# Kernel optimization log

Hardware: AMD Instinct MI355X
Metric: run time of the kernel (lower is better)

The kernel has to match this reference:

```python
import jax, jax.numpy as jnp
import numpy as np
import math

LEVELS = 10
T = 4096              # 2**log2_hashmap_size, log2=12
F = 2                 # n_features_per_level
NMIN, NMAX = 16, 320
HIDDEN = 512
OMEGA = 30.0
COOR_DIM = LEVELS * F + 2   # 22: hash feats + raw coords
_b = math.exp((math.log(NMAX) - math.log(NMIN)) / (LEVELS - 1))
RES = [int(math.floor(NMIN * _b ** l)) for l in range(LEVELS)]
PRIME_Y = np.uint32(2654435761)
MASK = np.uint32(T - 1)


def _hash2(xi, yi):
    # instant-NGP style spatial hash for 2D, uint32 wraparound arithmetic
    return (xi ^ (yi * PRIME_Y)) & MASK


def hash_encode(coords, table):
    # coords: [N,2] in [0,1); table: [LEVELS, T, F]
    feats = []
    for l in range(LEVELS):
        x = coords * RES[l]               # [N,2] continuous grid coords
        x0 = jnp.floor(x)
        w = x - x0                        # bilinear weights in [0,1)
        xi = x0.astype(jnp.uint32)
        x0i, y0i = xi[:, 0], xi[:, 1]
        x1i, y1i = x0i + np.uint32(1), y0i + np.uint32(1)
        tab = table[l]
        f00 = tab[_hash2(x0i, y0i)]       # [N,F] gathers
        f10 = tab[_hash2(x1i, y0i)]
        f01 = tab[_hash2(x0i, y1i)]
        f11 = tab[_hash2(x1i, y1i)]
        wx = w[:, 0:1]
        wy = w[:, 1:2]
        fx0 = f00 + (f10 - f00) * wx
        fx1 = f01 + (f11 - f01) * wx
        feats.append(fx0 + (fx1 - fx0) * wy)
    return jnp.concatenate(feats + [coords], axis=-1)  # [N, COOR_DIM]


def sine(x, w, b):
    # SineLayer.forward: sin(linear(x)); omega_0 is baked into first-layer init
    return jnp.sin(x @ w.T + b)


def _sine_init(key, out_f, in_f, is_first):
    kw, kb = jax.random.split(key)
    if is_first:
        lim = OMEGA / in_f
    else:
        lim = math.sqrt(6.0 / in_f) / OMEGA
    w = jax.random.uniform(kw, (out_f, in_f), jnp.float32, -lim, lim)
    blim = 1.0 / math.sqrt(in_f)
    b = jax.random.uniform(kb, (out_f,), jnp.float32, -blim, blim)
    return w, b


def setup_inputs() -> dict:
    key = jax.random.key(0)
    ks = jax.random.split(key, 8)
    N = 262144
    coords = jax.random.uniform(ks[0], (N, 2), jnp.float32)
    table = jax.random.uniform(ks[1], (LEVELS, T, F), jnp.float32, -1e-4, 1e-4)
    w1, b1 = _sine_init(ks[2], HIDDEN, COOR_DIM, True)
    w2, b2 = _sine_init(ks[3], HIDDEN, HIDDEN, False)
    ws1, bs1 = _sine_init(ks[4], HIDDEN, COOR_DIM + HIDDEN, False)
    ws2, bs2 = _sine_init(ks[5], HIDDEN, HIDDEN, False)
    wo, bo = _sine_init(ks[6], 2, HIDDEN, False)
    return {"coords": coords, "table": table,
            "w1": w1, "b1": b1, "w2": w2, "b2": b2,
            "ws1": ws1, "bs1": bs1, "ws2": ws2, "bs2": bs2,
            "wo": wo, "bo": bo}


def reference(coords, table, w1, b1, w2, b2, ws1, bs1, ws2, bs2, wo, bo):
    h0 = hash_encode(coords, table)            # [N,22]
    h1 = sine(sine(h0, w1, b1), w2, b2)        # first block (n_flayer=2)
    h2 = jnp.concatenate([h1, h0], axis=-1)    # skip connection [N,534]
    h2 = sine(sine(h2, ws1, bs1), ws2, bs2)    # second block (n_slayer=2)
    return sine(h2, wo, bo)                    # [N,2]
```

## Files before the change

### kernel.cpp

```cpp
#include <hip/hip_runtime.h>
#include <hip/hip_bf16.h>
#include <math.h>

#define MBLK    64
#define H0_OFF  65536
#define LDSB    (H0_OFF + 64*64)

#define OFF_W1  0
#define OFF_W2  16384
#define OFF_WS1 (16384+262144)
#define OFF_WS2 (278528+278528)
#define OFF_WO  (557056+262144)
#define NPACK   (819200+1024)

typedef __attribute__((ext_vector_type(8))) short bf16x8;
typedef __attribute__((ext_vector_type(4))) float f32x4;

struct ResArr { int r[10]; };

__device__ __forceinline__ unsigned short f2bf(float f) {
    unsigned u = __float_as_uint(f);
    u += 0x7FFFu + ((u >> 16) & 1u);
    return (unsigned short)(u >> 16);
}
__device__ __forceinline__ float bf2f(unsigned short h) {
    return __uint_as_float(((unsigned)h) << 16);
}

__global__ void pack_weights(const float* __restrict__ w1, const float* __restrict__ w2,
                             const float* __restrict__ ws1, const float* __restrict__ ws2,
                             const float* __restrict__ wo, unsigned short* __restrict__ out)
{
    int i = blockIdx.x * 256 + threadIdx.x;
    if (i >= NPACK) return;
    float v;
    if (i < OFF_WO) {
        int il, KC, K_src, K_valid;
        const float* src;
        if (i < OFF_W2)       { il = i;           KC = 1;  K_src = 22;  K_valid = 22;  src = w1;  }
        else if (i < OFF_WS1) { il = i - OFF_W2;  KC = 16; K_src = 512; K_valid = 512; src = w2;  }
        else if (i < OFF_WS2) { il = i - OFF_WS1; KC = 17; K_src = 534; K_valid = 534; src = ws1; }
        else                  { il = i - OFF_WS2; KC = 16; K_src = 512; K_valid = 512; src = ws2; }
        int blk  = il >> 9, idx = il & 511;
        int lane = idx >> 3, j = idx & 7;
        int nf   = blk & 3;
        int rest = blk >> 2;
        int c    = rest % KC;
        int nb   = rest / KC;
        int n = nb * 64 + nf * 16 + (lane & 15);
        int k = c * 32 + (lane >> 4) * 8 + j;
        v = (k < K_valid) ? src[n * K_src + k] : 0.f;
    } else {
        v = wo[i - OFF_WO];
    }
    out[i] = f2bf(v);
}

template<int KSTEPS, bool TAIL, bool PREBAR>
__device__ __forceinline__ void mlp_layer(char* sm, const unsigned short* __restrict__ Wl,
                                          const float* __restrict__ bias,
                                          int wid, int lane)
{
    constexpr int NC = KSTEPS + (TAIL ? 1 : 0);
    const int n0 = wid * 64;
    const int lm = lane & 15;
    const int lk = lane >> 4;
    const int xm = lm << 4;

    const unsigned short* wnb = Wl + (unsigned)(wid * NC) * 2048 + (lane << 3);

    f32x4 acc[4][4];
    #pragma unroll
    for (int i = 0; i < 4; ++i)
        #pragma unroll
        for (int j = 0; j < 4; ++j) { f32x4 z = {0.f,0.f,0.f,0.f}; acc[i][j] = z; }

    #pragma unroll 1
    for (int ks = 0; ks < KSTEPS; ++ks) {
        bf16x8 w[4], a[4];
        #pragma unroll
        for (int nf = 0; nf < 4; ++nf)
            w[nf] = *(const bf16x8*)(wnb + ((ks*4 + nf) << 9));
        #pragma unroll
        for (int mf = 0; mf < 4; ++mf)
            a[mf] = *(const bf16x8*)(sm + ((((mf*16 + lm) << 10) + ks*64 + lk*16) ^ xm));
        #pragma unroll
        for (int mf = 0; mf < 4; ++mf)
            #pragma unroll
            for (int nf = 0; nf < 4; ++nf)
                acc[mf][nf] = __builtin_amdgcn_mfma_f32_16x16x32_bf16(w[nf], a[mf], acc[mf][nf], 0, 0, 0);
    }
    if (TAIL) {
        bf16x8 w[4], a[4];
        #pragma unroll
        for (int nf = 0; nf < 4; ++nf)
            w[nf] = *(const bf16x8*)(wnb + ((KSTEPS*4 + nf) << 9));
        #pragma unroll
        for (int mf = 0; mf < 4; ++mf)
            a[mf] = *(const bf16x8*)(sm + H0_OFF + ((((mf*16 + lm) << 6) + lk*16) ^ ((lm & 7) << 4)));
        #pragma unroll
        for (int mf = 0; mf < 4; ++mf)
            #pragma unroll
            for (int nf = 0; nf < 4; ++nf)
                acc[mf][nf] = __builtin_amdgcn_mfma_f32_16x16x32_bf16(w[nf], a[mf], acc[mf][nf], 0, 0, 0);
    }

    if (PREBAR) __syncthreads();

    #pragma unroll
    for (int nf = 0; nf < 4; ++nf) {
        const float4 bv = *(const float4*)(bias + n0 + nf*16 + lk*4);
        const int colb = (n0 + nf*16 + lk*4) * 2;
        #pragma unroll
        for (int mf = 0; mf < 4; ++mf) {
            float s0 = __sinf(acc[mf][nf][0] + bv.x);
            float s1 = __sinf(acc[mf][nf][1] + bv.y);
            float s2 = __sinf(acc[mf][nf][2] + bv.z);
            float s3 = __sinf(acc[mf][nf][3] + bv.w);
            uint2 pk;
            pk.x = (unsigned)f2bf(s0) | ((unsigned)f2bf(s1) << 16);
            pk.y = (unsigned)f2bf(s2) | ((unsigned)f2bf(s3) << 16);
            int row = mf*16 + lm;
            *(uint2*)(sm + (((row << 10) + colb) ^ xm)) = pk;
        }
    }
    __syncthreads();
}

__global__ __launch_bounds__(512) __attribute__((amdgpu_waves_per_eu(4))) void siren_fused(
    const float* __restrict__ coords, const float* __restrict__ table,
    const float* __restrict__ b1, const float* __restrict__ b2,
    const float* __restrict__ bs1, const float* __restrict__ bs2,
    const float* __restrict__ bo,
    const unsigned short* __restrict__ Wp,
    float* __restrict__ outp,
    ResArr res)
{
    extern __shared__ char sm[];
    const int tid = threadIdx.x;
    const int pbase = blockIdx.x * MBLK;

    {
        int p  = tid & 63;
        int lg = tid >> 6;
        float2 cc = ((const float2*)coords)[pbase + p];
        #pragma unroll
        for (int li = 0; li < 2; ++li) {
            int l = lg + 8 * li;
            if (l < 10) {
                float R  = (float)res.r[l];
                float fx = cc.x * R, fy = cc.y * R;
                float x0 = floorf(fx), y0 = floorf(fy);
                float wx = fx - x0,  wy = fy - y0;
                unsigned xi = (unsigned)x0, yi = (unsigned)y0;
                unsigned yp  = yi * 2654435761u;
                unsigned yp1 = (yi + 1u) * 2654435761u;
                unsigned h00 = (xi        ^ yp ) & 4095u;
                unsigned h10 = ((xi + 1u) ^ yp ) & 4095u;
                unsigned h01 = (xi        ^ yp1) & 4095u;
                unsigned h11 = ((xi + 1u) ^ yp1) & 4095u;
                const float2* tl = (const float2*)(table + l * 8192);
                float2 f00 = tl[h00], f10 = tl[h10], f01 = tl[h01], f11 = tl[h11];
                float a0 = f00.x + (f10.x - f00.x) * wx;
                float a1 = f01.x + (f11.x - f01.x) * wx;
                float g0 = a0 + (a1 - a0) * wy;
                float c0 = f00.y + (f10.y - f00.y) * wx;
                float c1 = f01.y + (f11.y - f01.y) * wx;
                float g1 = c0 + (c1 - c0) * wy;
                unsigned pk = (unsigned)f2bf(g0) | ((unsigned)f2bf(g1) << 16);
                *(unsigned*)(sm + H0_OFF + (((p << 6) + 4*l) ^ ((p & 7) << 4))) = pk;
            }
        }
        if (lg == 2) {
            unsigned pk = (unsigned)f2bf(cc.x) | ((unsigned)f2bf(cc.y) << 16);
            *(unsigned*)(sm + H0_OFF + (((p << 6) + 40) ^ ((p & 7) << 4))) = pk;
        }
        if (lg == 3) {
            #pragma unroll
            for (int bb = 44; bb < 64; bb += 4)
                *(unsigned*)(sm + H0_OFF + (((p << 6) + bb) ^ ((p & 7) << 4))) = 0u;
        }
    }
    __syncthreads();

    const int wid  = tid >> 6;
    const int lane = tid & 63;

    mlp_layer<0,  true,  false>(sm, Wp + OFF_W1,  b1,  wid, lane);
    mlp_layer<16, false, true >(sm, Wp + OFF_W2,  b2,  wid, lane);
    mlp_layer<16, true,  true >(sm, Wp + OFF_WS1, bs1, wid, lane);
    mlp_layer<16, false, true >(sm, Wp + OFF_WS2, bs2, wid, lane);

    {
        int p = tid >> 3, g = tid & 7;
        const unsigned short* wo0 = Wp + OFF_WO + g * 64;
        const unsigned short* wo1 = wo0 + 512;
        int xm = (p & 15) << 4;
        float s0 = 0.f, s1 = 0.f;
        #pragma unroll
        for (int kk = 0; kk < 8; ++kk) {
            int off = ((p << 10) + g*128 + kk*16) ^ xm;
            bf16x8 av  = *(const bf16x8*)(sm + off);
            bf16x8 w0  = *(const bf16x8*)(wo0 + kk * 8);
            bf16x8 w1v = *(const bf16x8*)(wo1 + kk * 8);
            #pragma unroll
            for (int j = 0; j < 8; ++j) {
                float a = bf2f((unsigned short)av[j]);
                s0 += a * bf2f((unsigned short)w0[j]);
                s1 += a * bf2f((unsigned short)w1v[j]);
            }
        }
        #pragma unroll
        for (int m = 1; m < 8; m <<= 1) {
            s0 += __shfl_xor(s0, m, 64);
            s1 += __shfl_xor(s1, m, 64);
        }
        if (g == 0) {
            float2 o;
            o.x = __sinf(s0 + bo[0]);
            o.y = __sinf(s1 + bo[1]);
            ((float2*)outp)[pbase + p] = o;
        }
    }
}

extern "C" void kernel_launch(void* const* d_in, const int* in_sizes, int n_in,
                              void* d_out, int out_size, void* d_ws, size_t ws_size,
                              hipStream_t stream)
{
    const float* coords = (const float*)d_in[0];
    const float* table  = (const float*)d_in[1];
    const float* w1  = (const float*)d_in[2];
    const float* b1  = (const float*)d_in[3];
    const float* w2  = (const float*)d_in[4];
    const float* b2  = (const float*)d_in[5];
    const float* ws1 = (const float*)d_in[6];
    const float* bs1 = (const float*)d_in[7];
    const float* ws2 = (const float*)d_in[8];
    const float* bs2 = (const float*)d_in[9];
    const float* wo  = (const float*)d_in[10];
    const float* bo  = (const float*)d_in[11];

    unsigned short* Wp = (unsigned short*)d_ws;
    float* outp = (float*)d_out;

    ResArr res;
    double bb = exp((log(320.0) - log(16.0)) / 9.0);
    for (int l = 0; l < 10; ++l) res.r[l] = (int)floor(16.0 * pow(bb, (double)l));

    (void)hipFuncSetAttribute((const void*)siren_fused,
                              hipFuncAttributeMaxDynamicSharedMemorySize, LDSB);

    int N = in_sizes[0] / 2;

    pack_weights<<<(NPACK + 255) / 256, 256, 0, stream>>>(w1, w2, ws1, ws2, wo, Wp);
    siren_fused<<<N / MBLK, 512, LDSB, stream>>>(coords, table, b1, b2, bs1, bs2, bo,
                                                 Wp, outp, res);
}
```

Measured before the change: 414.3 us.

## Switch MLP layers from 16x16x32 to 32x32x16 bf16 MFMA tiles

Replaces the 4x4 grid of 16x16x32 MFMAs per wave with a 2x2 grid of 32x32x16 MFMAs, and repacks the weights to match the new operand layout. The larger MFMA shape halves the operand fragments loaded per instruction for the same 64x64 output tile, cutting LDS and global weight loads per FLOP. It also unrolls the K loop by 2 and changes the epilogue indexing to the 32x32 accumulator layout. The risks are a different LDS bank-conflict pattern under the 16-row swizzle and register pressure from the unroll.

```diff
diff --git a/kernel.cpp b/kernel.cpp
--- a/kernel.cpp
+++ b/kernel.cpp
@@ -13,8 +13,8 @@
 #define OFF_WO  (557056+262144)
 #define NPACK   (819200+1024)
 
-typedef __attribute__((ext_vector_type(8))) short bf16x8;
-typedef __attribute__((ext_vector_type(4))) float f32x4;
+typedef __attribute__((ext_vector_type(8)))  short bf16x8;
+typedef __attribute__((ext_vector_type(16))) float f32x16;
 
 struct ResArr { int r[10]; };
 
@@ -35,20 +35,20 @@
     if (i >= NPACK) return;
     float v;
     if (i < OFF_WO) {
-        int il, KC, K_src, K_valid;
+        int il, NC2, K_src, K_valid;
         const float* src;
-        if (i < OFF_W2)       { il = i;           KC = 1;  K_src = 22;  K_valid = 22;  src = w1;  }
-        else if (i < OFF_WS1) { il = i - OFF_W2;  KC = 16; K_src = 512; K_valid = 512; src = w2;  }
-        else if (i < OFF_WS2) { il = i - OFF_WS1; KC = 17; K_src = 534; K_valid = 534; src = ws1; }
-        else                  { il = i - OFF_WS2; KC = 16; K_src = 512; K_valid = 512; src = ws2; }
+        if (i < OFF_W2)       { il = i;           NC2 = 2;  K_src = 22;  K_valid = 22;  src = w1;  }
+        else if (i < OFF_WS1) { il = i - OFF_W2;  NC2 = 32; K_src = 512; K_valid = 512; src = w2;  }
+        else if (i < OFF_WS2) { il = i - OFF_WS1; NC2 = 34; K_src = 534; K_valid = 534; src = ws1; }
+        else                  { il = i - OFF_WS2; NC2 = 32; K_src = 512; K_valid = 512; src = ws2; }
         int blk  = il >> 9, idx = il & 511;
         int lane = idx >> 3, j = idx & 7;
-        int nf   = blk & 3;
-        int rest = blk >> 2;
-        int c    = rest % KC;
-        int nb   = rest / KC;
-        int n = nb * 64 + nf * 16 + (lane & 15);
-        int k = c * 32 + (lane >> 4) * 8 + j;
+        int nr   = blk & 1;
+        int rest = blk >> 1;
+        int c    = rest % NC2;
+        int nb   = rest / NC2;
+        int n = nb * 64 + nr * 32 + (lane & 31);
+        int k = c * 16 + (lane >> 5) * 8 + j;
         v = (k < K_valid) ? src[n * K_src + k] : 0.f;
     } else {
         v = wo[i - OFF_WO];
@@ -61,67 +61,80 @@
                                           const float* __restrict__ bias,
                                           int wid, int lane)
 {
-    constexpr int NC = KSTEPS + (TAIL ? 1 : 0);
-    const int n0 = wid * 64;
-    const int lm = lane & 15;
-    const int lk = lane >> 4;
-    const int xm = lm << 4;
-
-    const unsigned short* wnb = Wl + (unsigned)(wid * NC) * 2048 + (lane << 3);
-
-    f32x4 acc[4][4];
+    constexpr int NC2 = KSTEPS + (TAIL ? 2 : 0);
+    const int n0  = wid * 64;
+    const int l31 = lane & 31;
+    const int hi  = lane >> 5;
+
+    const unsigned short* wnb = Wl + (unsigned)(wid * NC2) * 1024 + (lane << 3);
+
+    f32x16 acc[2][2];
     #pragma unroll
-    for (int i = 0; i < 4; ++i)
-        #pragma unroll
-        for (int j = 0; j < 4; ++j) { f32x4 z = {0.f,0.f,0.f,0.f}; acc[i][j] = z; }
-
-    #pragma unroll 1
+    for (int mr = 0; mr < 2; ++mr)
+        #pragma unroll
+        for (int nr = 0; nr < 2; ++nr)
+            #pragma unroll
+            for (int e = 0; e < 16; ++e) acc[mr][nr][e] = 0.f;
+
+    #pragma unroll 2
     for (int ks = 0; ks < KSTEPS; ++ks) {
-        bf16x8 w[4], a[4];
-        #pragma unroll
-        for (int nf = 0; nf < 4; ++nf)
-            w[nf] = *(const bf16x8*)(wnb + ((ks*4 + nf) << 9));
-        #pragma unroll
-        for (int mf = 0; mf < 4; ++mf)
-            a[mf] = *(const bf16x8*)(sm + ((((mf*16 + lm) << 10) + ks*64 + lk*16) ^ xm));
-        #pragma unroll
-        for (int mf = 0; mf < 4; ++mf)
-            #pragma unroll
-            for (int nf = 0; nf < 4; ++nf)
-                acc[mf][nf] = __builtin_amdgcn_mfma_f32_16x16x32_bf16(w[nf], a[mf], acc[mf][nf], 0, 0, 0);
+        bf16x8 w[2], a[2];
+        #pragma unroll
+        for (int nr = 0; nr < 2; ++nr)
+            w[nr] = *(const bf16x8*)(wnb + ((ks*2 + nr) << 9));
+        #pragma unroll
+        for (int mr = 0; mr < 2; ++mr) {
+            int row = mr*32 + l31;
+            a[mr] = *(const bf16x8*)(sm + ((((row << 10) + ks*32 + hi*16)) ^ ((row & 15) << 4)));
+        }
+        #pragma unroll
+        for (int mr = 0; mr < 2; ++mr)
+            #pragma unroll
+            for (int nr = 0; nr < 2; ++nr)
+                acc[mr][nr] = __builtin_amdgcn_mfma_f32_32x32x16_bf16(w[nr], a[mr], acc[mr][nr], 0, 0, 0);
     }
     if (TAIL) {
-        bf16x8 w[4], a[4];
-        #pragma unroll
-        for (int nf = 0; nf < 4; ++nf)
-            w[nf] = *(const bf16x8*)(wnb + ((KSTEPS*4 + nf) << 9));
-        #pragma unroll
-        for (int mf = 0; mf < 4; ++mf)
-            a[mf] = *(const bf16x8*)(sm + H0_OFF + ((((mf*16 + lm) << 6) + lk*16) ^ ((lm & 7) << 4)));
-        #pragma unroll
-        for (int mf = 0; mf < 4; ++mf)
-            #pragma unroll
-            for (int nf = 0; nf < 4; ++nf)
-                acc[mf][nf] = __builtin_amdgcn_mfma_f32_16x16x32_bf16(w[nf], a[mf], acc[mf][nf], 0, 0, 0);
+        #pragma unroll
+        for (int kt = 0; kt < 2; ++kt) {
+            bf16x8 w[2], a[2];
+            #pragma unroll
+            for (int nr = 0; nr < 2; ++nr)
+                w[nr] = *(const bf16x8*)(wnb + (((KSTEPS + kt)*2 + nr) << 9));
+            #pragma unroll
+            for (int mr = 0; mr < 2; ++mr) {
+                int row = mr*32 + l31;
+                a[mr] = *(const bf16x8*)(sm + H0_OFF + ((((row << 6) + kt*32 + hi*16)) ^ ((row & 7) << 4)));
+            }
+            #pragma unroll
+            for (int mr = 0; mr < 2; ++mr)
+                #pragma unroll
+                for (int nr = 0; nr < 2; ++nr)
+                    acc[mr][nr] = __builtin_amdgcn_mfma_f32_32x32x16_bf16(w[nr], a[mr], acc[mr][nr], 0, 0, 0);
+        }
     }
 
     if (PREBAR) __syncthreads();
 
     #pragma unroll
-    for (int nf = 0; nf < 4; ++nf) {
-        const float4 bv = *(const float4*)(bias + n0 + nf*16 + lk*4);
-        const int colb = (n0 + nf*16 + lk*4) * 2;
-        #pragma unroll
-        for (int mf = 0; mf < 4; ++mf) {
-            float s0 = __sinf(acc[mf][nf][0] + bv.x);
-            float s1 = __sinf(acc[mf][nf][1] + bv.y);
-            float s2 = __sinf(acc[mf][nf][2] + bv.z);
-            float s3 = __sinf(acc[mf][nf][3] + bv.w);
-            uint2 pk;
-            pk.x = (unsigned)f2bf(s0) | ((unsigned)f2bf(s1) << 16);
-            pk.y = (unsigned)f2bf(s2) | ((unsigned)f2bf(s3) << 16);
-            int row = mf*16 + lm;
-            *(uint2*)(sm + (((row << 10) + colb) ^ xm)) = pk;
+    for (int mr = 0; mr < 2; ++mr) {
+        const int m    = mr*32 + l31;
+        const int rowb = m << 10;
+        const int sw   = (m & 15) << 4;
+        #pragma unroll
+        for (int nr = 0; nr < 2; ++nr) {
+            #pragma unroll
+            for (int q = 0; q < 4; ++q) {
+                const int nb4 = n0 + nr*32 + q*8 + hi*4;
+                const float4 bv = *(const float4*)(bias + nb4);
+                float s0 = __sinf(acc[mr][nr][q*4+0] + bv.x);
+                float s1 = __sinf(acc[mr][nr][q*4+1] + bv.y);
+                float s2 = __sinf(acc[mr][nr][q*4+2] + bv.z);
+                float s3 = __sinf(acc[mr][nr][q*4+3] + bv.w);
+                uint2 pk;
+                pk.x = (unsigned)f2bf(s0) | ((unsigned)f2bf(s1) << 16);
+                pk.y = (unsigned)f2bf(s2) | ((unsigned)f2bf(s3) << 16);
+                *(uint2*)(sm + ((rowb + nb4*2) ^ sw)) = pk;
+            }
         }
     }
     __syncthreads();
@@ -187,9 +200,9 @@
     const int lane = tid & 63;
 
     mlp_layer<0,  true,  false>(sm, Wp + OFF_W1,  b1,  wid, lane);
-    mlp_layer<16, false, true >(sm, Wp + OFF_W2,  b2,  wid, lane);
-    mlp_layer<16, true,  true >(sm, Wp + OFF_WS1, bs1, wid, lane);
-    mlp_layer<16, false, true >(sm, Wp + OFF_WS2, bs2, wid, lane);
+    mlp_layer<32, false, true >(sm, Wp + OFF_W2,  b2,  wid, lane);
+    mlp_layer<32, true,  true >(sm, Wp + OFF_WS1, bs1, wid, lane);
+    mlp_layer<32, false, true >(sm, Wp + OFF_WS2, bs2, wid, lane);
 
     {
         int p = tid >> 3, g = tid & 7;
```

Measured after the change: 461.5 us. 11.4% more time.
